# Performance work log

Measured on AMD Instinct MI355X. Metric: run time of the kernel, lower is better.

Reference implementation:

```python
import jax, jax.numpy as jnp
import numpy as np

B, S, D, E, H = 4, 2048, 1024, 8, 4096  # batch, seq, d_model, n_experts, ffn hidden (4*d_model)


def setup_inputs() -> dict:
    key = jax.random.key(0)
    ks = jax.random.split(key, 4)
    s = 0.02  # init scale
    return {
        "x": jax.random.normal(ks[0], (B, S, D), dtype=jnp.float32),
        "router_w": jax.random.normal(ks[1], (E, D), dtype=jnp.float32) * s,
        "router_b": jnp.zeros((E,), dtype=jnp.float32),
        "w1": jax.random.normal(ks[2], (E, D, H), dtype=jnp.float32) * s,
        "b1": jnp.zeros((E, H), dtype=jnp.float32),
        "w2": jax.random.normal(ks[3], (E, H, D), dtype=jnp.float32) * s,
        "b2": jnp.zeros((E, D), dtype=jnp.float32),
        "top_k": 2,
    }


def reference(x, router_w, router_b, w1, b1, w2, b2, top_k):
    # Router logits [B, S, E]
    logits = jnp.einsum('bsd,ed->bse', x, router_w) + router_b
    # Top-k selection; scatter top-k logits into a -inf tensor, then softmax
    # => gate weight is exactly 0 for non-selected experts.
    top_v, top_i = jax.lax.top_k(logits, top_k)           # [B, S, k]
    sel = jax.nn.one_hot(top_i, logits.shape[-1], dtype=bool).any(axis=-2)  # [B, S, E]
    gate = jax.nn.softmax(jnp.where(sel, logits, -jnp.inf), axis=-1)        # [B, S, E]

    # Dense sum over experts (mathematically identical to the masked
    # gather/scatter loop since non-selected gates are exactly 0).
    out = jnp.zeros_like(x)
    for e in range(w1.shape[0]):  # small fixed expert loop keeps peak memory low
        h = jax.nn.relu(x @ w1[e] + b1[e])        # [B, S, H]
        out = out + (h @ w2[e] + b2[e]) * gate[..., e:e + 1]
    return out
```

## Files before the change

### kernel.cpp

```cpp
#include <hip/hip_runtime.h>
#include <hip/hip_bf16.h>

#define NTOK   8192
#define DMODEL 1024
#define NEXP   8
#define HFFN   4096
#define NSLOT  16384
#define MAXWL  72

typedef __bf16 bf16x8 __attribute__((ext_vector_type(8)));
typedef float  f32x4  __attribute__((ext_vector_type(4)));
typedef unsigned short u16;
typedef u16 u16x8 __attribute__((ext_vector_type(8)));

typedef const __attribute__((address_space(1))) void* gas_ptr;
typedef __attribute__((address_space(3))) void* las_ptr;

__device__ inline u16 f2b(float f) {
  __hip_bfloat16 h = __float2bfloat16(f);
  return *reinterpret_cast<u16*>(&h);
}
__device__ inline float b2f(u16 u) {
  unsigned int v = ((unsigned int)u) << 16;
  return *reinterpret_cast<float*>(&v);
}

__global__ void router_k(const float* __restrict__ x, const float* __restrict__ rw,
                         const float* __restrict__ rb, int* __restrict__ tok_e,
                         float* __restrict__ tok_g) {
  int wave = threadIdx.x >> 6, lane = threadIdx.x & 63;
  int t = blockIdx.x * 4 + wave;
  const float* xr = x + (size_t)t * DMODEL;
  float acc[NEXP];
#pragma unroll
  for (int e = 0; e < NEXP; e++) acc[e] = 0.f;
#pragma unroll
  for (int i = 0; i < 4; i++) {
    int d = i * 256 + lane * 4;
    float4 xv = *(const float4*)(xr + d);
#pragma unroll
    for (int e = 0; e < NEXP; e++) {
      float4 wv = *(const float4*)(rw + (size_t)e * DMODEL + d);
      acc[e] += xv.x * wv.x + xv.y * wv.y + xv.z * wv.z + xv.w * wv.w;
    }
  }
#pragma unroll
  for (int e = 0; e < NEXP; e++) {
#pragma unroll
    for (int off = 32; off > 0; off >>= 1) acc[e] += __shfl_xor(acc[e], off);
  }
  if (lane == 0) {
    float lg[NEXP];
#pragma unroll
    for (int e = 0; e < NEXP; e++) lg[e] = acc[e] + rb[e];
    int e0 = 0;
#pragma unroll
    for (int e = 1; e < NEXP; e++) if (lg[e] > lg[e0]) e0 = e;
    int e1 = (e0 == 0) ? 1 : 0;
#pragma unroll
    for (int e = 0; e < NEXP; e++) if (e != e0 && lg[e] > lg[e1]) e1 = e;
    float ex = expf(lg[e1] - lg[e0]);
    float g0 = 1.f / (1.f + ex);
    float g1 = ex / (1.f + ex);
    tok_e[2 * t]     = e0;  tok_e[2 * t + 1] = e1;
    tok_g[2 * t]     = g0;  tok_g[2 * t + 1] = g1;
  }
}

__global__ void count_k(const int* __restrict__ tok_e, int* __restrict__ counts) {
  __shared__ int h[NEXP];
  int tid = threadIdx.x;
  if (tid < NEXP) h[tid] = 0;
  __syncthreads();
  int t = blockIdx.x * 256 + tid;
  atomicAdd(&h[tok_e[2 * t]], 1);
  atomicAdd(&h[tok_e[2 * t + 1]], 1);
  __syncthreads();
  if (tid < NEXP) atomicAdd(&counts[tid], h[tid]);
}

__global__ void offsets_k(const int* __restrict__ counts, int* __restrict__ offsets,
                          int* __restrict__ wl) {
  if (threadIdx.x == 0) {
    int s = 0;
    for (int e = 0; e < NEXP; e++) { offsets[e] = s; s += counts[e]; }
    offsets[NEXP] = s;
    int n = 0;
    for (int e = 0; e < NEXP; e++)
      for (int t = 0; t * 256 < counts[e]; ++t) wl[n++] = (e << 16) | t;
    for (int i = n; i < MAXWL; ++i) wl[i] = -1;
  }
}

__global__ void assign_k(const int* __restrict__ tok_e, int* __restrict__ cursors,
                         const int* __restrict__ offsets, int* __restrict__ row_tok,
                         int* __restrict__ slot_of) {
  __shared__ int h[NEXP], base[NEXP];
  int tid = threadIdx.x;
  if (tid < NEXP) h[tid] = 0;
  __syncthreads();
  int t = blockIdx.x * 256 + tid;
  int e0 = tok_e[2 * t], e1 = tok_e[2 * t + 1];
  int r0 = atomicAdd(&h[e0], 1);
  int r1 = atomicAdd(&h[e1], 1);
  __syncthreads();
  if (tid < NEXP) base[tid] = atomicAdd(&cursors[tid], h[tid]);
  __syncthreads();
  int s0 = offsets[e0] + base[e0] + r0;
  int s1 = offsets[e1] + base[e1] + r1;
  row_tok[s0] = t;  slot_of[2 * t] = s0;
  row_tok[s1] = t;  slot_of[2 * t + 1] = s1;
}

__global__ void gather_k(const float* __restrict__ x, const int* __restrict__ row_tok,
                         u16* __restrict__ xbg) {
  int idx = blockIdx.x * 256 + threadIdx.x;
  int s = idx >> 8;
  int c = (idx & 255) * 4;
  int t = row_tok[s];
  float4 v = *(const float4*)(x + (size_t)t * DMODEL + c);
  ushort4 o;
  o.x = f2b(v.x); o.y = f2b(v.y); o.z = f2b(v.z); o.w = f2b(v.w);
  *(ushort4*)(xbg + (size_t)s * DMODEL + c) = o;
}

__global__ void wtrans_k(const float* __restrict__ src, u16* __restrict__ dst,
                         int R, int C) {
  __shared__ u16 tile[64][72];
  int e = blockIdx.z;
  int r0 = blockIdx.x * 64, c0 = blockIdx.y * 64;
  int tid = threadIdx.x;
  int tr = tid >> 2, tc = (tid & 3) * 16;
  const float* sp = src + (size_t)e * R * C + (size_t)(r0 + tr) * C + c0 + tc;
#pragma unroll
  for (int i = 0; i < 16; i += 4) {
    float4 v = *(const float4*)(sp + i);
    tile[tr][tc + i]     = f2b(v.x);
    tile[tr][tc + i + 1] = f2b(v.y);
    tile[tr][tc + i + 2] = f2b(v.z);
    tile[tr][tc + i + 3] = f2b(v.w);
  }
  __syncthreads();
  u16* dbase = dst + (size_t)e * R * C;
#pragma unroll
  for (int it = 0; it < 2; ++it) {
    int oc  = it * 32 + (tid >> 3);
    int seg = (tid & 7) * 8;
    u16x8 o;
#pragma unroll
    for (int j = 0; j < 8; ++j) o[j] = tile[seg + j][oc];
    *(u16x8*)(dbase + (size_t)(c0 + oc) * R + r0 + seg) = o;
  }
}

template <int KTOT, int KCHUNK, int NTOT, int NY, int NKQ, bool RELU, bool BIAS>
__global__ __launch_bounds__(512, 2) void moe_gemm_k(
    const u16* __restrict__ A, const u16* __restrict__ Bt,
    const float* __restrict__ bias, u16* __restrict__ Out,
    const int* __restrict__ counts, const int* __restrict__ offsets,
    const int* __restrict__ wl) {
  __shared__ __align__(16) u16 Als[3 * 8192];
  __shared__ __align__(16) u16 Bls[3 * 8192];

  int nwg = gridDim.x;
  int lid = blockIdx.x;
  int orig = (lid & 7) * (nwg >> 3) + (lid >> 3);
  int kq   = orig / (MAXWL * NY);
  int r1   = orig - kq * (MAXWL * NY);
  int pair = r1 / (MAXWL * 2);
  int r2   = r1 - pair * (MAXWL * 2);
  int xt = r2 >> 1;
  int y  = (pair << 1) | (r2 & 1);
  int w = wl[xt];
  if (w < 0) return;
  int e   = w >> 16;
  int tr0 = (w & 0xffff) << 8;
  int cnt = counts[e];
  int seg = offsets[e];
  int n0  = y << 8;

  int tid = threadIdx.x;
  int wid = tid >> 6, lane = tid & 63;
  int wm = wid >> 2, wn = wid & 3;
  int l15 = lane & 15, lhi = lane >> 4;

  int co = (((tid & 3) ^ ((tid >> 3) & 3)) << 3) + kq * KCHUNK;
  const u16* gA[2]; const u16* gB[2];
  const u16* Bte = Bt + (size_t)e * NTOT * KTOT;
#pragma unroll
  for (int j = 0; j < 2; ++j) {
    gA[j] = A + (size_t)(seg + tr0 + j * 128 + (tid >> 2)) * KTOT + co;
    gB[j] = Bte + (size_t)(n0 + j * 128 + (tid >> 2)) * KTOT + co;
  }
  char* Ab = (char*)Als;
  char* Bb = (char*)Bls;
  int sdst = wid << 10;

  auto stage = [&](int bs, int kb) {
#pragma unroll
    for (int j = 0; j < 2; ++j) {
      __builtin_amdgcn_global_load_lds((gas_ptr)(gA[j] + kb),
          (las_ptr)(Ab + bs * 16384 + j * 8192 + sdst), 16, 0, 0);
      __builtin_amdgcn_global_load_lds((gas_ptr)(gB[j] + kb),
          (las_ptr)(Bb + bs * 16384 + j * 8192 + sdst), 16, 0, 0);
    }
  };

  int xsw = ((lhi ^ ((l15 >> 1) & 3)) << 4);
  int aoff = (wm * 128 + l15) * 64 + xsw;
  int boff = (wn * 64 + l15) * 64 + xsw;

  constexpr int NT = KCHUNK / 32;

  stage(0, 0);
  stage(1, 32);
  asm volatile("s_waitcnt vmcnt(4)" ::: "memory");
  __builtin_amdgcn_s_barrier();
  __builtin_amdgcn_sched_barrier(0);

  f32x4 acc[8][4] = {};
  int bufC = 0;
  for (int T = 0; T < NT; ++T) {
    int bufS = bufC + 2; if (bufS >= 3) bufS -= 3;
    bool ds = (T + 2 < NT);
    const char* ab = Ab + bufC * 16384;
    const char* bb = Bb + bufC * 16384;
    bf16x8 af[4], bv[4];

#pragma unroll
    for (int n = 0; n < 4; ++n) bv[n] = *(const bf16x8*)(bb + boff + n * 1024);
#pragma unroll
    for (int m = 0; m < 4; ++m) af[m] = *(const bf16x8*)(ab + aoff + m * 1024);
    if (ds) stage(bufS, (T + 2) * 32);
    __builtin_amdgcn_s_setprio(1);
#pragma unroll
    for (int m = 0; m < 4; ++m)
#pragma unroll
      for (int n = 0; n < 4; ++n)
        acc[m][n] = __builtin_amdgcn_mfma_f32_16x16x32_bf16(af[m], bv[n], acc[m][n], 0, 0, 0);
    __builtin_amdgcn_s_setprio(0);

#pragma unroll
    for (int m = 0; m < 4; ++m) af[m] = *(const bf16x8*)(ab + aoff + (4 + m) * 1024);
    __builtin_amdgcn_s_setprio(1);
#pragma unroll
    for (int m = 0; m < 4; ++m)
#pragma unroll
      for (int n = 0; n < 4; ++n)
        acc[4 + m][n] = __builtin_amdgcn_mfma_f32_16x16x32_bf16(af[m], bv[n], acc[4 + m][n], 0, 0, 0);
    __builtin_amdgcn_s_setprio(0);

    if (T + 1 < NT) {
      if (ds) asm volatile("s_waitcnt vmcnt(4)" ::: "memory");
      else    asm volatile("s_waitcnt vmcnt(0)" ::: "memory");
      __builtin_amdgcn_s_barrier();
      __builtin_amdgcn_sched_barrier(0);
    }
    bufC += 1; if (bufC >= 3) bufC -= 3;
  }

  u16* outp = Out + (size_t)kq * ((size_t)NSLOT * NTOT);

  int cb = n0 + wn * 64 + l15;
  float bs4[4] = {0.f, 0.f, 0.f, 0.f};
  if (BIAS) {
    const float* bias_e = bias + (size_t)e * NTOT;
#pragma unroll
    for (int n = 0; n < 4; ++n) bs4[n] = bias_e[cb + n * 16];
  }
  int rb0 = tr0 + wm * 128 + lhi * 4;
#pragma unroll
  for (int m = 0; m < 8; ++m) {
#pragma unroll
    for (int r = 0; r < 4; ++r) {
      int gi = rb0 + m * 16 + r;
      if (gi >= cnt) continue;
      size_t orow = (size_t)(seg + gi) * NTOT + cb;
#pragma unroll
      for (int n = 0; n < 4; ++n) {
        float v = acc[m][n][r] + bs4[n];
        if (RELU) v = fmaxf(v, 0.f);
        outp[orow + n * 16] = f2b(v);
      }
    }
  }
}

__global__ void combine_k(const u16* __restrict__ Y, const int* __restrict__ slot_of,
                          const int* __restrict__ tok_e, const float* __restrict__ tok_g,
                          const float* __restrict__ b2, float* __restrict__ out) {
  int t = blockIdx.x;
  int d = threadIdx.x * 4;
  int s0 = slot_of[2 * t], s1 = slot_of[2 * t + 1];
  int e0 = tok_e[2 * t],  e1 = tok_e[2 * t + 1];
  float g0 = tok_g[2 * t], g1 = tok_g[2 * t + 1];
  const u16* Y1 = Y + (size_t)NSLOT * DMODEL;
  ushort4 a0 = *(const ushort4*)(Y  + (size_t)s0 * DMODEL + d);
  ushort4 a1 = *(const ushort4*)(Y1 + (size_t)s0 * DMODEL + d);
  ushort4 c0 = *(const ushort4*)(Y  + (size_t)s1 * DMODEL + d);
  ushort4 c1 = *(const ushort4*)(Y1 + (size_t)s1 * DMODEL + d);
  float4 b20 = *(const float4*)(b2 + (size_t)e0 * DMODEL + d);
  float4 b21 = *(const float4*)(b2 + (size_t)e1 * DMODEL + d);
  float4 o;
  o.x = g0 * (b2f(a0.x) + b2f(a1.x) + b20.x) + g1 * (b2f(c0.x) + b2f(c1.x) + b21.x);
  o.y = g0 * (b2f(a0.y) + b2f(a1.y) + b20.y) + g1 * (b2f(c0.y) + b2f(c1.y) + b21.y);
  o.z = g0 * (b2f(a0.z) + b2f(a1.z) + b20.z) + g1 * (b2f(c0.z) + b2f(c1.z) + b21.z);
  o.w = g0 * (b2f(a0.w) + b2f(a1.w) + b20.w) + g1 * (b2f(c0.w) + b2f(c1.w) + b21.w);
  *(float4*)(out + (size_t)t * DMODEL + d) = o;
}

extern "C" void kernel_launch(void* const* d_in, const int* in_sizes, int n_in,
                              void* d_out, int out_size, void* d_ws, size_t ws_size,
                              hipStream_t stream) {
  const float* x  = (const float*)d_in[0];
  const float* rw = (const float*)d_in[1];
  const float* rb = (const float*)d_in[2];
  const float* w1 = (const float*)d_in[3];
  const float* b1 = (const float*)d_in[4];
  const float* w2 = (const float*)d_in[5];
  const float* b2 = (const float*)d_in[6];

  char* ws = (char*)d_ws;
  size_t o = 0;
  u16* w1t = (u16*)(ws + o); o += (size_t)NEXP * HFFN * DMODEL * 2;
  u16* w2t = (u16*)(ws + o); o += (size_t)NEXP * HFFN * DMODEL * 2;
  u16* xbg = (u16*)(ws + o); o += (size_t)(NSLOT + 256) * DMODEL * 2;
  u16* hc  = (u16*)(ws + o); o += (size_t)(NSLOT + 256) * HFFN * 2;
  u16* yp  = (u16*)w1t;
  int*   tok_e   = (int*)(ws + o);   o += NTOK * 2 * sizeof(int);
  float* tok_g   = (float*)(ws + o); o += NTOK * 2 * sizeof(float);
  int*   slot_of = (int*)(ws + o);   o += NTOK * 2 * sizeof(int);
  int*   row_tok = (int*)(ws + o);   o += NSLOT * sizeof(int);
  int*   meta    = (int*)(ws + o);   o += 32 * sizeof(int);
  int*   wl      = (int*)(ws + o);   o += MAXWL * sizeof(int);
  int* counts  = meta;
  int* cursors = meta + 8;
  int* offsets = meta + 16;

  hipMemsetAsync(meta, 0, 64, stream);
  router_k<<<NTOK / 4, 256, 0, stream>>>(x, rw, rb, tok_e, tok_g);
  count_k<<<NTOK / 256, 256, 0, stream>>>(tok_e, counts);
  offsets_k<<<1, 64, 0, stream>>>(counts, offsets, wl);
  assign_k<<<NTOK / 256, 256, 0, stream>>>(tok_e, cursors, offsets, row_tok, slot_of);
  gather_k<<<NSLOT, 256, 0, stream>>>(x, row_tok, xbg);
  wtrans_k<<<dim3(DMODEL / 64, HFFN / 64, NEXP), 256, 0, stream>>>(w1, w1t, DMODEL, HFFN);
  wtrans_k<<<dim3(HFFN / 64, DMODEL / 64, NEXP), 256, 0, stream>>>(w2, w2t, HFFN, DMODEL);

  moe_gemm_k<DMODEL, DMODEL, HFFN, HFFN / 256, 1, true, true>
      <<<MAXWL * (HFFN / 256), 512, 0, stream>>>(
          xbg, w1t, b1, hc, counts, offsets, wl);
  moe_gemm_k<HFFN, HFFN / 2, DMODEL, DMODEL / 256, 2, false, false>
      <<<MAXWL * (DMODEL / 256) * 2, 512, 0, stream>>>(
          hc, w2t, nullptr, yp, counts, offsets, wl);

  combine_k<<<NTOK, 256, 0, stream>>>(yp, slot_of, tok_e, tok_g, b2, (float*)d_out);
}
```

Measured before the change: 588.8 us.

## Shrink MoE GEMM tiles to 128x128, drop LDS pipelining, fuse expert counting into router

The expert GEMM tile shrinks from 256x256 with 512 threads and a 3-stage LDS pipeline to 128x128 with 256 threads and a single-buffered load/wait/compute loop. The work list becomes 128-row tiles (MAXWL 136) to match. Separately, the per-expert histogram moves into the router kernel, removing the count_k launch. The smaller tiles cut padding waste on partial expert tiles and allow more blocks per CU, but they give up load/compute overlap and halve data reuse per tile.

```diff
diff --git a/kernel.cpp b/kernel.cpp
--- a/kernel.cpp
+++ b/kernel.cpp
@@ -6,7 +6,7 @@
 #define NEXP   8
 #define HFFN   4096
 #define NSLOT  16384
-#define MAXWL  72
+#define MAXWL  136
 
 typedef __bf16 bf16x8 __attribute__((ext_vector_type(8)));
 typedef float  f32x4  __attribute__((ext_vector_type(4)));
@@ -27,8 +27,12 @@
 
 __global__ void router_k(const float* __restrict__ x, const float* __restrict__ rw,
                          const float* __restrict__ rb, int* __restrict__ tok_e,
-                         float* __restrict__ tok_g) {
-  int wave = threadIdx.x >> 6, lane = threadIdx.x & 63;
+                         float* __restrict__ tok_g, int* __restrict__ counts) {
+  __shared__ int h[NEXP];
+  int tid = threadIdx.x;
+  if (tid < NEXP) h[tid] = 0;
+  __syncthreads();
+  int wave = tid >> 6, lane = tid & 63;
   int t = blockIdx.x * 4 + wave;
   const float* xr = x + (size_t)t * DMODEL;
   float acc[NEXP];
@@ -64,19 +68,11 @@
     float g1 = ex / (1.f + ex);
     tok_e[2 * t]     = e0;  tok_e[2 * t + 1] = e1;
     tok_g[2 * t]     = g0;  tok_g[2 * t + 1] = g1;
-  }
-}
-
-__global__ void count_k(const int* __restrict__ tok_e, int* __restrict__ counts) {
-  __shared__ int h[NEXP];
-  int tid = threadIdx.x;
-  if (tid < NEXP) h[tid] = 0;
-  __syncthreads();
-  int t = blockIdx.x * 256 + tid;
-  atomicAdd(&h[tok_e[2 * t]], 1);
-  atomicAdd(&h[tok_e[2 * t + 1]], 1);
-  __syncthreads();
-  if (tid < NEXP) atomicAdd(&counts[tid], h[tid]);
+    atomicAdd(&h[e0], 1);
+    atomicAdd(&h[e1], 1);
+  }
+  __syncthreads();
+  if (tid < NEXP && h[tid]) atomicAdd(&counts[tid], h[tid]);
 }
 
 __global__ void offsets_k(const int* __restrict__ counts, int* __restrict__ offsets,
@@ -87,7 +83,7 @@
     offsets[NEXP] = s;
     int n = 0;
     for (int e = 0; e < NEXP; e++)
-      for (int t = 0; t * 256 < counts[e]; ++t) wl[n++] = (e << 16) | t;
+      for (int t = 0; t * 128 < counts[e]; ++t) wl[n++] = (e << 16) | t;
     for (int i = n; i < MAXWL; ++i) wl[i] = -1;
   }
 }
@@ -153,14 +149,14 @@
   }
 }
 
-template <int KTOT, int KCHUNK, int NTOT, int NY, int NKQ, bool RELU, bool BIAS>
-__global__ __launch_bounds__(512, 2) void moe_gemm_k(
+template <int KTOT, int KCHUNK, int NTOT, int NY, bool RELU, bool BIAS>
+__global__ __launch_bounds__(256, 4) void moe_gemm_k(
     const u16* __restrict__ A, const u16* __restrict__ Bt,
     const float* __restrict__ bias, u16* __restrict__ Out,
     const int* __restrict__ counts, const int* __restrict__ offsets,
     const int* __restrict__ wl) {
-  __shared__ __align__(16) u16 Als[3 * 8192];
-  __shared__ __align__(16) u16 Bls[3 * 8192];
+  __shared__ __align__(16) u16 Als[128 * 32];
+  __shared__ __align__(16) u16 Bls[128 * 32];
 
   int nwg = gridDim.x;
   int lid = blockIdx.x;
@@ -174,89 +170,52 @@
   int w = wl[xt];
   if (w < 0) return;
   int e   = w >> 16;
-  int tr0 = (w & 0xffff) << 8;
+  int tr0 = (w & 0xffff) << 7;
   int cnt = counts[e];
   int seg = offsets[e];
-  int n0  = y << 8;
+  int n0  = y << 7;
 
   int tid = threadIdx.x;
   int wid = tid >> 6, lane = tid & 63;
-  int wm = wid >> 2, wn = wid & 3;
+  int wm = wid >> 1, wn = wid & 1;
   int l15 = lane & 15, lhi = lane >> 4;
 
   int co = (((tid & 3) ^ ((tid >> 3) & 3)) << 3) + kq * KCHUNK;
-  const u16* gA[2]; const u16* gB[2];
+  const u16* gA0 = A + (size_t)(seg + tr0 + (tid >> 2)) * KTOT + co;
+  const u16* gA1 = gA0 + (size_t)64 * KTOT;
   const u16* Bte = Bt + (size_t)e * NTOT * KTOT;
-#pragma unroll
-  for (int j = 0; j < 2; ++j) {
-    gA[j] = A + (size_t)(seg + tr0 + j * 128 + (tid >> 2)) * KTOT + co;
-    gB[j] = Bte + (size_t)(n0 + j * 128 + (tid >> 2)) * KTOT + co;
-  }
+  const u16* gB0 = Bte + (size_t)(n0 + (tid >> 2)) * KTOT + co;
+  const u16* gB1 = gB0 + (size_t)64 * KTOT;
   char* Ab = (char*)Als;
   char* Bb = (char*)Bls;
   int sdst = wid << 10;
 
-  auto stage = [&](int bs, int kb) {
-#pragma unroll
-    for (int j = 0; j < 2; ++j) {
-      __builtin_amdgcn_global_load_lds((gas_ptr)(gA[j] + kb),
-          (las_ptr)(Ab + bs * 16384 + j * 8192 + sdst), 16, 0, 0);
-      __builtin_amdgcn_global_load_lds((gas_ptr)(gB[j] + kb),
-          (las_ptr)(Bb + bs * 16384 + j * 8192 + sdst), 16, 0, 0);
-    }
-  };
-
   int xsw = ((lhi ^ ((l15 >> 1) & 3)) << 4);
-  int aoff = (wm * 128 + l15) * 64 + xsw;
+  int aoff = (wm * 64 + l15) * 64 + xsw;
   int boff = (wn * 64 + l15) * 64 + xsw;
 
+  f32x4 acc[4][4] = {};
   constexpr int NT = KCHUNK / 32;
-
-  stage(0, 0);
-  stage(1, 32);
-  asm volatile("s_waitcnt vmcnt(4)" ::: "memory");
-  __builtin_amdgcn_s_barrier();
-  __builtin_amdgcn_sched_barrier(0);
-
-  f32x4 acc[8][4] = {};
-  int bufC = 0;
-  for (int T = 0; T < NT; ++T) {
-    int bufS = bufC + 2; if (bufS >= 3) bufS -= 3;
-    bool ds = (T + 2 < NT);
-    const char* ab = Ab + bufC * 16384;
-    const char* bb = Bb + bufC * 16384;
+  for (int kt = 0; kt < NT; ++kt) {
+    int kb = kt * 32;
+    __builtin_amdgcn_global_load_lds((gas_ptr)(gA0 + kb), (las_ptr)(Ab + sdst), 16, 0, 0);
+    __builtin_amdgcn_global_load_lds((gas_ptr)(gA1 + kb), (las_ptr)(Ab + 4096 + sdst), 16, 0, 0);
+    __builtin_amdgcn_global_load_lds((gas_ptr)(gB0 + kb), (las_ptr)(Bb + sdst), 16, 0, 0);
+    __builtin_amdgcn_global_load_lds((gas_ptr)(gB1 + kb), (las_ptr)(Bb + 4096 + sdst), 16, 0, 0);
+    asm volatile("s_waitcnt vmcnt(0)" ::: "memory");
+    __builtin_amdgcn_s_barrier();
+
     bf16x8 af[4], bv[4];
-
-#pragma unroll
-    for (int n = 0; n < 4; ++n) bv[n] = *(const bf16x8*)(bb + boff + n * 1024);
-#pragma unroll
-    for (int m = 0; m < 4; ++m) af[m] = *(const bf16x8*)(ab + aoff + m * 1024);
-    if (ds) stage(bufS, (T + 2) * 32);
-    __builtin_amdgcn_s_setprio(1);
+#pragma unroll
+    for (int m = 0; m < 4; ++m) af[m] = *(const bf16x8*)(Ab + aoff + m * 1024);
+#pragma unroll
+    for (int n = 0; n < 4; ++n) bv[n] = *(const bf16x8*)(Bb + boff + n * 1024);
 #pragma unroll
     for (int m = 0; m < 4; ++m)
 #pragma unroll
       for (int n = 0; n < 4; ++n)
         acc[m][n] = __builtin_amdgcn_mfma_f32_16x16x32_bf16(af[m], bv[n], acc[m][n], 0, 0, 0);
-    __builtin_amdgcn_s_setprio(0);
-
-#pragma unroll
-    for (int m = 0; m < 4; ++m) af[m] = *(const bf16x8*)(ab + aoff + (4 + m) * 1024);
-    __builtin_amdgcn_s_setprio(1);
-#pragma unroll
-    for (int m = 0; m < 4; ++m)
-#pragma unroll
-      for (int n = 0; n < 4; ++n)
-        acc[4 + m][n] = __builtin_amdgcn_mfma_f32_16x16x32_bf16(af[m], bv[n], acc[4 + m][n], 0, 0, 0);
-    __builtin_amdgcn_s_setprio(0);
-
-    if (T + 1 < NT) {
-      if (ds) asm volatile("s_waitcnt vmcnt(4)" ::: "memory");
-      else    asm volatile("s_waitcnt vmcnt(0)" ::: "memory");
-      __builtin_amdgcn_s_barrier();
-      __builtin_amdgcn_sched_barrier(0);
-    }
-    bufC += 1; if (bufC >= 3) bufC -= 3;
+    __builtin_amdgcn_s_barrier();
   }
 
   u16* outp = Out + (size_t)kq * ((size_t)NSLOT * NTOT);
@@ -268,9 +227,9 @@
 #pragma unroll
     for (int n = 0; n < 4; ++n) bs4[n] = bias_e[cb + n * 16];
   }
-  int rb0 = tr0 + wm * 128 + lhi * 4;
-#pragma unroll
-  for (int m = 0; m < 8; ++m) {
+  int rb0 = tr0 + wm * 64 + lhi * 4;
+#pragma unroll
+  for (int m = 0; m < 4; ++m) {
 #pragma unroll
     for (int r = 0; r < 4; ++r) {
       int gi = rb0 + m * 16 + r;
@@ -338,19 +297,18 @@
   int* offsets = meta + 16;
 
   hipMemsetAsync(meta, 0, 64, stream);
-  router_k<<<NTOK / 4, 256, 0, stream>>>(x, rw, rb, tok_e, tok_g);
-  count_k<<<NTOK / 256, 256, 0, stream>>>(tok_e, counts);
+  router_k<<<NTOK / 4, 256, 0, stream>>>(x, rw, rb, tok_e, tok_g, counts);
   offsets_k<<<1, 64, 0, stream>>>(counts, offsets, wl);
   assign_k<<<NTOK / 256, 256, 0, stream>>>(tok_e, cursors, offsets, row_tok, slot_of);
   gather_k<<<NSLOT, 256, 0, stream>>>(x, row_tok, xbg);
   wtrans_k<<<dim3(DMODEL / 64, HFFN / 64, NEXP), 256, 0, stream>>>(w1, w1t, DMODEL, HFFN);
   wtrans_k<<<dim3(HFFN / 64, DMODEL / 64, NEXP), 256, 0, stream>>>(w2, w2t, HFFN, DMODEL);
 
-  moe_gemm_k<DMODEL, DMODEL, HFFN, HFFN / 256, 1, true, true>
-      <<<MAXWL * (HFFN / 256), 512, 0, stream>>>(
+  moe_gemm_k<DMODEL, DMODEL, HFFN, HFFN / 128, true, true>
+      <<<MAXWL * (HFFN / 128), 256, 0, stream>>>(
           xbg, w1t, b1, hc, counts, offsets, wl);
-  moe_gemm_k<HFFN, HFFN / 2, DMODEL, DMODEL / 256, 2, false, false>
-      <<<MAXWL * (DMODEL / 256) * 2, 512, 0, stream>>>(
+  moe_gemm_k<HFFN, HFFN / 2, DMODEL, DMODEL / 128, false, false>
+      <<<MAXWL * (DMODEL / 128) * 2, 256, 0, stream>>>(
           hc, w2t, nullptr, yp, counts, offsets, wl);
 
   combine_k<<<NTOK, 256, 0, stream>>>(yp, slot_of, tok_e, tok_g, b2, (float*)d_out);
```

After: 527.2 us. -10.5%, faster.
